# Kernel tuning notes

Measured on AMD Instinct MI355X. Metric: run time of the kernel, lower is better.

## Reference

```python
import jax, jax.numpy as jnp
import numpy as np

LN_EPS = 1e-5

def _ln(x, w, b):
    mu = jnp.mean(x, axis=-1, keepdims=True)
    var = jnp.var(x, axis=-1, keepdims=True)
    return (x - mu) * jax.lax.rsqrt(var + LN_EPS) * w + b

def setup_inputs() -> dict:
    key = jax.random.key(0)
    ks = jax.random.split(key, 16)
    B, T, N = 32, 1024, 77
    D, TD, TE = 512, 256, 2048
    s = lambda fan: 1.0 / np.sqrt(fan)
    return {
        "x": jax.random.normal(ks[0], (B, T, D), jnp.float32),
        "xf": jax.random.normal(ks[1], (B, N, TD), jnp.float32),
        "emb": jax.random.normal(ks[2], (B, TE), jnp.float32),
        "src_mask": jnp.ones((B, T), jnp.float32),
        "cond_type": jax.random.randint(ks[3], (B,), 0, 100, jnp.int64),
        "norm_w": jnp.ones((D,), jnp.float32),
        "norm_b": jnp.zeros((D,), jnp.float32),
        "tnorm_w": jnp.ones((TD,), jnp.float32),
        "tnorm_b": jnp.zeros((TD,), jnp.float32),
        "Wq": jax.random.normal(ks[4], (D, D), jnp.float32) * s(D),
        "bq": jnp.zeros((D,), jnp.float32),
        "Wk": jax.random.normal(ks[5], (D, TD), jnp.float32) * s(TD),
        "bk": jnp.zeros((D,), jnp.float32),
        "Wv": jax.random.normal(ks[6], (D, TD), jnp.float32) * s(TD),
        "bv": jnp.zeros((D,), jnp.float32),
        "emb_w": jax.random.normal(ks[7], (2 * D, TE), jnp.float32) * s(TE),
        "emb_b": jnp.zeros((2 * D,), jnp.float32),
        "snorm_w": jnp.ones((D,), jnp.float32),
        "snorm_b": jnp.zeros((D,), jnp.float32),
        "Wout": jax.random.normal(ks[8], (D, D), jnp.float32) * s(D),
        "bout": jnp.zeros((D,), jnp.float32),
    }

def reference(x, xf, emb, src_mask, cond_type,
              norm_w, norm_b, tnorm_w, tnorm_b,
              Wq, bq, Wk, bk, Wv, bv,
              emb_w, emb_b, snorm_w, snorm_b, Wout, bout):
    B, T, D = x.shape
    N = xf.shape[1]
    H = 8
    dh = D // H
    # projections (no 1/sqrt(dh) scaling, per original)
    q = (_ln(x, norm_w, norm_b) @ Wq.T + bq).reshape(B, T, H, dh)
    xf_n = _ln(xf, tnorm_w, tnorm_b)
    k = (xf_n @ Wk.T + bk).reshape(B, N, H, dh)
    # cond_type gating: text_cond_type = (cond_type % 10 > 0)
    tc = (cond_type % 10 > 0).astype(x.dtype)  # [B]
    bias = (1.0 - tc)[:, None, None, None] * -1000000.0  # [B,1,1,1]
    attn = jnp.einsum('bthd,bnhd->btnh', q, k) + bias
    attn = jax.nn.softmax(attn, axis=2)  # over keys N
    v = (xf_n @ Wv.T + bv) * tc[:, None, None]
    v = v.reshape(B, N, H, dh)
    y = jnp.einsum('btnh,bnhd->bthd', attn, v).reshape(B, T, D)
    # StylizationBlock: silu->linear on emb -> scale/shift, ln, silu->linear, residual
    e = jax.nn.silu(emb) @ emb_w.T + emb_b  # [B, 2D]
    scale, shift = jnp.split(e[:, None, :], 2, axis=2)  # [B,1,D] each
    h = _ln(y, snorm_w, snorm_b) * (1.0 + scale) + shift
    h = jax.nn.silu(h) @ Wout.T + bout
    return x + h
```

## Files before the change

### kernel.cpp

```cpp
#include <hip/hip_runtime.h>
#include <math.h>

#define B_   32
#define T_   1024
#define N_   77
#define D_   512
#define TD_  256
#define TE_  2048
#define H_   8
#define DH_  64

typedef short bf16x8 __attribute__((ext_vector_type(8)));
typedef float f32x4  __attribute__((ext_vector_type(4)));

__device__ __forceinline__ float sigmoidf_fast(float x) {
    return 1.0f / (1.0f + __expf(-x));
}

__device__ __forceinline__ unsigned short f2b(float f) {
    unsigned int u = __float_as_uint(f);
    unsigned int r = u + 0x7FFFu + ((u >> 16) & 1u);
    return (unsigned short)(r >> 16);
}

#define GL16(g, l) __builtin_amdgcn_global_load_lds(                         \
    (const __attribute__((address_space(1))) unsigned int*)(g),              \
    (__attribute__((address_space(3))) unsigned int*)(l), 16, 0, 0)

__global__ __launch_bounds__(256) void ln_xf_kernel(
    const float* __restrict__ x, const float* __restrict__ w, const float* __restrict__ b,
    unsigned short* __restrict__ outb)
{
    int row = blockIdx.x * 4 + (threadIdx.x >> 6);
    int lane = threadIdx.x & 63;
    const float* rp = x + (size_t)row * TD_ + lane * 4;
    float4 v = *(const float4*)rp;
    float s  = v.x + v.y + v.z + v.w;
    float ss = v.x*v.x + v.y*v.y + v.z*v.z + v.w*v.w;
    #pragma unroll
    for (int off = 32; off; off >>= 1) {
        s  += __shfl_xor(s, off);
        ss += __shfl_xor(ss, off);
    }
    float m = s * (1.f / TD_);
    float r = rsqrtf(ss * (1.f / TD_) - m * m + 1e-5f);
    float4 wv = *(const float4*)(w + lane * 4);
    float4 bv = *(const float4*)(b + lane * 4);
    ushort4 o;
    o.x = f2b((v.x - m) * r * wv.x + bv.x);
    o.y = f2b((v.y - m) * r * wv.y + bv.y);
    o.z = f2b((v.z - m) * r * wv.z + bv.z);
    o.w = f2b((v.w - m) * r * wv.w + bv.w);
    *(ushort4*)(outb + (size_t)row * TD_ + lane * 4) = o;
}

__global__ __launch_bounds__(256) void conv_weights_kernel(
    const float* __restrict__ Wq, const float* __restrict__ Wout,
    const float* __restrict__ Wk, const float* __restrict__ Wv,
    unsigned short* __restrict__ wqb, unsigned short* __restrict__ wob,
    unsigned short* __restrict__ wkvb)
{
    int bid = blockIdx.x;
    const float* src; unsigned short* dst;
    if (bid < 128)      { src = Wq;   dst = wqb; }
    else if (bid < 256) { src = Wout; dst = wob;               bid -= 128; }
    else if (bid < 320) { src = Wk;   dst = wkvb;              bid -= 256; }
    else                { src = Wv;   dst = wkvb + D_ * TD_;   bid -= 320; }
    int idx = (bid * 256 + threadIdx.x) * 8;
    float4 v0 = *(const float4*)(src + idx);
    float4 v1 = *(const float4*)(src + idx + 4);
    ushort4 o0 = {f2b(v0.x), f2b(v0.y), f2b(v0.z), f2b(v0.w)};
    ushort4 o1 = {f2b(v1.x), f2b(v1.y), f2b(v1.z), f2b(v1.w)};
    *(ushort4*)(dst + idx)     = o0;
    *(ushort4*)(dst + idx + 4) = o1;
}

__global__ __launch_bounds__(256) void kv_gemm_kernel(
    const unsigned short* __restrict__ Ab,
    const unsigned short* __restrict__ Wb,
    const float* __restrict__ bkp, const float* __restrict__ bvp,
    const int*   __restrict__ cond,
    unsigned short* __restrict__ kout, unsigned short* __restrict__ vout)
{
    constexpr int K = TD_;
    __shared__ __align__(16) unsigned short As[128 * 32];
    __shared__ __align__(16) unsigned short Bs[128 * 32];

    const int tid  = threadIdx.x;
    const int m0   = blockIdx.y * 128;
    const int n0   = blockIdx.x * 128;
    const int lane = tid & 63;
    const int w    = tid >> 6;
    const int l15  = lane & 15;
    const int quad = lane >> 4;
    const int wm   = (w >> 1) * 64;
    const int wn   = (w & 1) * 64;

    const int row_a = tid >> 2;
    const int col16 = tid & 3;

    f32x4 acc[4][4];
    #pragma unroll
    for (int i = 0; i < 4; i++)
        #pragma unroll
        for (int j = 0; j < 4; j++)
            acc[i][j] = (f32x4){0.f, 0.f, 0.f, 0.f};

    const char* gAbase = (const char*)Ab + ((size_t)(m0 + row_a) * K) * 2 + col16 * 16;
    const char* gBbase = (const char*)Wb + ((size_t)(n0 + row_a) * K) * 2 + col16 * 16;
    char* lA = (char*)As + tid * 16;
    char* lB = (char*)Bs + tid * 16;

    for (int k0 = 0; k0 < K; k0 += 32) {
        const char* gA = gAbase + k0 * 2;
        const char* gB = gBbase + k0 * 2;
        GL16(gA, lA);
        GL16(gA + (size_t)64 * K * 2, lA + 4096);
        GL16(gB, lB);
        GL16(gB + (size_t)64 * K * 2, lB + 4096);
        __syncthreads();

        bf16x8 af[4], bfr[4];
        #pragma unroll
        for (int i = 0; i < 4; i++)
            af[i] = *(const bf16x8*)&As[(wm + i * 16 + l15) * 32 + quad * 8];
        #pragma unroll
        for (int j = 0; j < 4; j++)
            bfr[j] = *(const bf16x8*)&Bs[(wn + j * 16 + l15) * 32 + quad * 8];
        #pragma unroll
        for (int i = 0; i < 4; i++)
            #pragma unroll
            for (int j = 0; j < 4; j++)
                acc[i][j] = __builtin_amdgcn_mfma_f32_16x16x32_bf16(af[i], bfr[j], acc[i][j], 0, 0, 0);
        __syncthreads();
    }

    #pragma unroll
    for (int i = 0; i < 4; i++) {
        int mbase = m0 + wm + i * 16 + quad * 4;
        #pragma unroll
        for (int j = 0; j < 4; j++) {
            int n = n0 + wn + j * 16 + l15;
            bool isv = n >= D_;
            int nn = isv ? n - D_ : n;
            float bn = isv ? bvp[nn] : bkp[nn];
            unsigned short* outp = isv ? vout : kout;
            #pragma unroll
            for (int r = 0; r < 4; r++) {
                int m = mbase + r;
                if (m >= B_ * N_) continue;
                float v = acc[i][j][r] + bn;
                if (isv) {
                    int bi = m / N_;
                    v = ((cond[bi] % 10) > 0) ? v : 0.f;
                }
                outp[(size_t)m * D_ + nn] = f2b(v);
            }
        }
    }
}

__global__ __launch_bounds__(256) void emb_gemm_kernel(
    const float* __restrict__ emb, const float* __restrict__ W,
    float* __restrict__ e)
{
    int wid = blockIdx.x * 4 + (threadIdx.x >> 6);
    int lane = threadIdx.x & 63;
    int ngrp = wid >> 3;
    int bgrp = wid & 7;

    float acc[4][4] = {};
    #pragma unroll 2
    for (int it = 0; it < 8; it++) {
        int k = (it * 64 + lane) * 4;
        float4 sv[4], wv[4];
        #pragma unroll
        for (int bi = 0; bi < 4; bi++) {
            float4 t = *(const float4*)&emb[(size_t)(bgrp * 4 + bi) * TE_ + k];
            t.x *= sigmoidf_fast(t.x);
            t.y *= sigmoidf_fast(t.y);
            t.z *= sigmoidf_fast(t.z);
            t.w *= sigmoidf_fast(t.w);
            sv[bi] = t;
        }
        #pragma unroll
        for (int ni = 0; ni < 4; ni++)
            wv[ni] = *(const float4*)&W[(size_t)(ngrp * 4 + ni) * TE_ + k];
        #pragma unroll
        for (int bi = 0; bi < 4; bi++)
            #pragma unroll
            for (int ni = 0; ni < 4; ni++) {
                acc[bi][ni] = fmaf(sv[bi].x, wv[ni].x, acc[bi][ni]);
                acc[bi][ni] = fmaf(sv[bi].y, wv[ni].y, acc[bi][ni]);
                acc[bi][ni] = fmaf(sv[bi].z, wv[ni].z, acc[bi][ni]);
                acc[bi][ni] = fmaf(sv[bi].w, wv[ni].w, acc[bi][ni]);
            }
    }
    #pragma unroll
    for (int bi = 0; bi < 4; bi++)
        #pragma unroll
        for (int ni = 0; ni < 4; ni++) {
            float a = acc[bi][ni];
            #pragma unroll
            for (int off = 32; off; off >>= 1) a += __shfl_xor(a, off);
            if (lane == 0)
                e[(size_t)(bgrp * 4 + bi) * 1024 + ngrp * 4 + ni] = a;
        }
}

__global__ __launch_bounds__(256) void prep_q_kernel(
    const float* __restrict__ x, const float* __restrict__ w, const float* __restrict__ b,
    unsigned short* __restrict__ outb)
{
    int row = blockIdx.x * 4 + (threadIdx.x >> 6);
    int lane = threadIdx.x & 63;
    const float* rp = x + (size_t)row * D_ + lane * 8;
    float4 v0 = *(const float4*)rp;
    float4 v1 = *(const float4*)(rp + 4);
    float s  = v0.x + v0.y + v0.z + v0.w + v1.x + v1.y + v1.z + v1.w;
    float ss = v0.x*v0.x + v0.y*v0.y + v0.z*v0.z + v0.w*v0.w
             + v1.x*v1.x + v1.y*v1.y + v1.z*v1.z + v1.w*v1.w;
    #pragma unroll
    for (int off = 32; off; off >>= 1) {
        s  += __shfl_xor(s, off);
        ss += __shfl_xor(ss, off);
    }
    float m = s * (1.f / D_);
    float r = rsqrtf(ss * (1.f / D_) - m * m + 1e-5f);
    float4 w0 = *(const float4*)(w + lane * 8);
    float4 w1 = *(const float4*)(w + lane * 8 + 4);
    float4 b0 = *(const float4*)(b + lane * 8);
    float4 b1 = *(const float4*)(b + lane * 8 + 4);
    ushort4 o0, o1;
    o0.x = f2b((v0.x - m) * r * w0.x + b0.x);
    o0.y = f2b((v0.y - m) * r * w0.y + b0.y);
    o0.z = f2b((v0.z - m) * r * w0.z + b0.z);
    o0.w = f2b((v0.w - m) * r * w0.w + b0.w);
    o1.x = f2b((v1.x - m) * r * w1.x + b1.x);
    o1.y = f2b((v1.y - m) * r * w1.y + b1.y);
    o1.z = f2b((v1.z - m) * r * w1.z + b1.z);
    o1.w = f2b((v1.w - m) * r * w1.w + b1.w);
    unsigned short* op = outb + (size_t)row * D_ + lane * 8;
    *(ushort4*)op       = o0;
    *(ushort4*)(op + 4) = o1;
}

__global__ __launch_bounds__(256) void prep_h_kernel(
    const float* __restrict__ y, const float* __restrict__ w, const float* __restrict__ b,
    const float* __restrict__ e, const float* __restrict__ emb_b,
    unsigned short* __restrict__ outb)
{
    int row = blockIdx.x * 4 + (threadIdx.x >> 6);
    int lane = threadIdx.x & 63;
    int bb = row >> 10;
    const float* rp = y + (size_t)row * D_ + lane * 8;
    float4 v0 = *(const float4*)rp;
    float4 v1 = *(const float4*)(rp + 4);
    float s  = v0.x + v0.y + v0.z + v0.w + v1.x + v1.y + v1.z + v1.w;
    float ss = v0.x*v0.x + v0.y*v0.y + v0.z*v0.z + v0.w*v0.w
             + v1.x*v1.x + v1.y*v1.y + v1.z*v1.z + v1.w*v1.w;
    #pragma unroll
    for (int off = 32; off; off >>= 1) {
        s  += __shfl_xor(s, off);
        ss += __shfl_xor(ss, off);
    }
    float m = s * (1.f / D_);
    float r = rsqrtf(ss * (1.f / D_) - m * m + 1e-5f);
    float4 w0 = *(const float4*)(w + lane * 8);
    float4 w1 = *(const float4*)(w + lane * 8 + 4);
    float4 b0 = *(const float4*)(b + lane * 8);
    float4 b1 = *(const float4*)(b + lane * 8 + 4);
    const float* ep = e + (size_t)bb * 1024 + lane * 8;
    float4 sc0 = *(const float4*)ep;
    float4 sc1 = *(const float4*)(ep + 4);
    float4 sh0 = *(const float4*)(ep + 512);
    float4 sh1 = *(const float4*)(ep + 512 + 4);
    float4 eb0 = *(const float4*)(emb_b + lane * 8);
    float4 eb1 = *(const float4*)(emb_b + lane * 8 + 4);
    float4 fb0 = *(const float4*)(emb_b + 512 + lane * 8);
    float4 fb1 = *(const float4*)(emb_b + 512 + lane * 8 + 4);
    sc0.x += eb0.x; sc0.y += eb0.y; sc0.z += eb0.z; sc0.w += eb0.w;
    sc1.x += eb1.x; sc1.y += eb1.y; sc1.z += eb1.z; sc1.w += eb1.w;
    sh0.x += fb0.x; sh0.y += fb0.y; sh0.z += fb0.z; sh0.w += fb0.w;
    sh1.x += fb1.x; sh1.y += fb1.y; sh1.z += fb1.z; sh1.w += fb1.w;
    float hv[8];
    hv[0] = ((v0.x - m) * r * w0.x + b0.x) * (1.f + sc0.x) + sh0.x;
    hv[1] = ((v0.y - m) * r * w0.y + b0.y) * (1.f + sc0.y) + sh0.y;
    hv[2] = ((v0.z - m) * r * w0.z + b0.z) * (1.f + sc0.z) + sh0.z;
    hv[3] = ((v0.w - m) * r * w0.w + b0.w) * (1.f + sc0.w) + sh0.w;
    hv[4] = ((v1.x - m) * r * w1.x + b1.x) * (1.f + sc1.x) + sh1.x;
    hv[5] = ((v1.y - m) * r * w1.y + b1.y) * (1.f + sc1.y) + sh1.y;
    hv[6] = ((v1.z - m) * r * w1.z + b1.z) * (1.f + sc1.z) + sh1.z;
    hv[7] = ((v1.w - m) * r * w1.w + b1.w) * (1.f + sc1.w) + sh1.w;
    ushort4 o0, o1;
    o0.x = f2b(hv[0] * sigmoidf_fast(hv[0]));
    o0.y = f2b(hv[1] * sigmoidf_fast(hv[1]));
    o0.z = f2b(hv[2] * sigmoidf_fast(hv[2]));
    o0.w = f2b(hv[3] * sigmoidf_fast(hv[3]));
    o1.x = f2b(hv[4] * sigmoidf_fast(hv[4]));
    o1.y = f2b(hv[5] * sigmoidf_fast(hv[5]));
    o1.z = f2b(hv[6] * sigmoidf_fast(hv[6]));
    o1.w = f2b(hv[7] * sigmoidf_fast(hv[7]));
    unsigned short* op = outb + (size_t)row * D_ + lane * 8;
    *(ushort4*)op       = o0;
    *(ushort4*)(op + 4) = o1;
}

template <int RESID, int OUTBF>
__global__ __launch_bounds__(256) void gemm_bf16_kernel(
    const unsigned short* __restrict__ Ab,
    const unsigned short* __restrict__ Wb,
    const float* __restrict__ bias,
    const float* __restrict__ resid,
    void* __restrict__ Cv)
{
    constexpr int K = 512;
    __shared__ __align__(16) unsigned short As[128 * 32];
    __shared__ __align__(16) unsigned short Bs[128 * 32];

    const int tid  = threadIdx.x;
    const int m0   = blockIdx.y * 128;
    const int n0   = blockIdx.x * 128;
    const int lane = tid & 63;
    const int w    = tid >> 6;
    const int l15  = lane & 15;
    const int quad = lane >> 4;
    const int wm   = (w >> 1) * 64;
    const int wn   = (w & 1) * 64;

    const int row_a = tid >> 2;
    const int col16 = tid & 3;

    f32x4 acc[4][4];
    #pragma unroll
    for (int i = 0; i < 4; i++)
        #pragma unroll
        for (int j = 0; j < 4; j++)
            acc[i][j] = (f32x4){0.f, 0.f, 0.f, 0.f};

    const char* gAbase = (const char*)Ab + ((size_t)(m0 + row_a) * K) * 2 + col16 * 16;
    const char* gBbase = (const char*)Wb + ((size_t)(n0 + row_a) * K) * 2 + col16 * 16;
    char* lA = (char*)As + tid * 16;
    char* lB = (char*)Bs + tid * 16;

    for (int k0 = 0; k0 < K; k0 += 32) {
        const char* gA = gAbase + k0 * 2;
        const char* gB = gBbase + k0 * 2;
        GL16(gA, lA);
        GL16(gA + (size_t)64 * K * 2, lA + 4096);
        GL16(gB, lB);
        GL16(gB + (size_t)64 * K * 2, lB + 4096);
        __syncthreads();

        bf16x8 af[4], bfr[4];
        #pragma unroll
        for (int i = 0; i < 4; i++)
            af[i] = *(const bf16x8*)&As[(wm + i * 16 + l15) * 32 + quad * 8];
        #pragma unroll
        for (int j = 0; j < 4; j++)
            bfr[j] = *(const bf16x8*)&Bs[(wn + j * 16 + l15) * 32 + quad * 8];
        #pragma unroll
        for (int i = 0; i < 4; i++)
            #pragma unroll
            for (int j = 0; j < 4; j++)
                acc[i][j] = __builtin_amdgcn_mfma_f32_16x16x32_bf16(af[i], bfr[j], acc[i][j], 0, 0, 0);
        __syncthreads();
    }

    float* C = (float*)Cv;
    unsigned short* Cb = (unsigned short*)Cv;
    #pragma unroll
    for (int i = 0; i < 4; i++) {
        int mbase = m0 + wm + i * 16 + quad * 4;
        #pragma unroll
        for (int j = 0; j < 4; j++) {
            int n = n0 + wn + j * 16 + l15;
            float bn = bias[n];
            #pragma unroll
            for (int r = 0; r < 4; r++) {
                size_t off = (size_t)(mbase + r) * 512 + n;
                float v = acc[i][j][r] + bn;
                if (RESID) v += resid[off];
                if (OUTBF) Cb[off] = f2b(v);
                else       C[off]  = v;
            }
        }
    }
}

#define KS2   0
#define VT2   5760
#define PS2   11904
#define SMEM2 18560

__global__ __launch_bounds__(256) void attn_mfma2_kernel(
    const unsigned short* __restrict__ qb,
    const unsigned short* __restrict__ kb,
    const unsigned short* __restrict__ vb,
    float* __restrict__ yout)
{
    __shared__ __align__(16) unsigned short smem[SMEM2];

    const int tid = threadIdx.x;
    const int t0 = blockIdx.x * 64;
    const int h  = blockIdx.y;
    const int b  = blockIdx.z;

    const int lane = tid & 63;
    const int w    = tid >> 6;
    const int l15  = lane & 15;
    const int quad = lane >> 4;
    const int koff = quad * 8;
    const int mrow = w * 16 + l15;

    const unsigned short* qrow = qb + ((size_t)(b * T_ + t0 + mrow)) * D_ + h * 64 + koff;
    bf16x8 aq0 = *(const bf16x8*)qrow;
    bf16x8 aq1 = *(const bf16x8*)(qrow + 32);

    const unsigned short* kbase = kb + ((size_t)(b * N_)) * D_ + h * 64;
    #pragma unroll
    for (int i = 0; i < 3; i++) {
        int idx = tid + i * 256;
        if (idx < 640) {
            int row = idx >> 3, c8 = idx & 7;
            bf16x8 v = (bf16x8){0, 0, 0, 0, 0, 0, 0, 0};
            if (row < N_) v = *(const bf16x8*)(kbase + (size_t)row * D_ + c8 * 8);
            *(bf16x8*)&smem[KS2 + row * 72 + c8 * 8] = v;
        }
    }
    const unsigned short* vbase = vb + ((size_t)(b * N_)) * D_ + h * 64;
    #pragma unroll
    for (int i = 0; i < 3; i++) {
        int idx = tid + i * 256;
        if (idx < 616) {
            int n = idx >> 3, c8 = idx & 7;
            bf16x8 v = *(const bf16x8*)(vbase + (size_t)n * D_ + c8 * 8);
            int cn = n >> 3, wn = n & 7;
            #pragma unroll
            for (int j = 0; j < 8; j++) {
                int d = c8 * 8 + j;
                int s2 = (j ^ c8) & 3;
                smem[VT2 + d * 96 + ((cn ^ s2) << 3) + wn] = v[j];
            }
        }
    }
    if (tid < 128) {
        int d = tid >> 1, c = 10 + (tid & 1);
        int s2 = (d ^ (d >> 3)) & 3;
        *(bf16x8*)&smem[VT2 + d * 96 + ((c ^ s2) << 3)] = (bf16x8){0, 0, 0, 0, 0, 0, 0, 0};
    }
    {
        int d = tid >> 2, t = tid & 3;
        if (t < 3) {
            int s2 = (d ^ (d >> 3)) & 3;
            smem[VT2 + d * 96 + ((9 ^ s2) << 3) + 5 + t] = 0;
        }
    }
    #pragma unroll
    for (int i = 0; i < 4; i++) {
        int idx = tid + i * 256;
        int row = idx >> 4, col = 80 + (idx & 15);
        smem[PS2 + row * 104 + col] = 0;
    }
    __syncthreads();

    float s[5][4];
    #pragma unroll
    for (int nt = 0; nt < 5; nt++) {
        bf16x8 bk0 = *(const bf16x8*)&smem[KS2 + (nt * 16 + l15) * 72 + koff];
        bf16x8 bk1 = *(const bf16x8*)&smem[KS2 + (nt * 16 + l15) * 72 + 32 + koff];
        f32x4 c = {0.f, 0.f, 0.f, 0.f};
        c = __builtin_amdgcn_mfma_f32_16x16x32_bf16(aq0, bk0, c, 0, 0, 0);
        c = __builtin_amdgcn_mfma_f32_16x16x32_bf16(aq1, bk1, c, 0, 0, 0);
        #pragma unroll
        for (int r = 0; r < 4; r++) s[nt][r] = c[r];
    }
    if (l15 >= N_ - 64) {
        #pragma unroll
        for (int r = 0; r < 4; r++) s[4][r] = -1e30f;
    }
    float li[4];
    #pragma unroll
    for (int r = 0; r < 4; r++) {
        float m = s[0][r];
        #pragma unroll
        for (int nt = 1; nt < 5; nt++) m = fmaxf(m, s[nt][r]);
        m = fmaxf(m, __shfl_xor(m, 1));
        m = fmaxf(m, __shfl_xor(m, 2));
        m = fmaxf(m, __shfl_xor(m, 4));
        m = fmaxf(m, __shfl_xor(m, 8));
        float l = 0.f;
        #pragma unroll
        for (int nt = 0; nt < 5; nt++) {
            float ev = __expf(s[nt][r] - m);
            s[nt][r] = ev;
            l += ev;
        }
        l += __shfl_xor(l, 1);
        l += __shfl_xor(l, 2);
        l += __shfl_xor(l, 4);
        l += __shfl_xor(l, 8);
        li[r] = 1.f / l;
    }
    #pragma unroll
    for (int r = 0; r < 4; r++) {
        int prow = w * 16 + quad * 4 + r;
        #pragma unroll
        for (int nt = 0; nt < 5; nt++) {
            smem[PS2 + prow * 104 + nt * 16 + l15] = f2b(s[nt][r] * li[r]);
        }
    }

    bf16x8 pa0 = *(const bf16x8*)&smem[PS2 + mrow * 104 + 0  + koff];
    bf16x8 pa1 = *(const bf16x8*)&smem[PS2 + mrow * 104 + 32 + koff];
    bf16x8 pa2 = *(const bf16x8*)&smem[PS2 + mrow * 104 + 64 + koff];

    float* obase = yout + ((size_t)(b * T_ + t0 + w * 16)) * D_ + h * 64;
    #pragma unroll
    for (int dt = 0; dt < 4; dt++) {
        int drow = dt * 16 + l15;
        int s2 = (drow ^ (drow >> 3)) & 3;
        bf16x8 bv0 = *(const bf16x8*)&smem[VT2 + drow * 96 + (((0 + quad) ^ s2) << 3)];
        bf16x8 bv1 = *(const bf16x8*)&smem[VT2 + drow * 96 + (((4 + quad) ^ s2) << 3)];
        bf16x8 bv2 = *(const bf16x8*)&smem[VT2 + drow * 96 + (((8 + quad) ^ s2) << 3)];
        f32x4 c = {0.f, 0.f, 0.f, 0.f};
        c = __builtin_amdgcn_mfma_f32_16x16x32_bf16(pa0, bv0, c, 0, 0, 0);
        c = __builtin_amdgcn_mfma_f32_16x16x32_bf16(pa1, bv1, c, 0, 0, 0);
        c = __builtin_amdgcn_mfma_f32_16x16x32_bf16(pa2, bv2, c, 0, 0, 0);
        #pragma unroll
        for (int r = 0; r < 4; r++) {
            obase[(size_t)(quad * 4 + r) * D_ + dt * 16 + l15] = c[r];
        }
    }
}

extern "C" void kernel_launch(void* const* d_in, const int* in_sizes, int n_in,
                              void* d_out, int out_size, void* d_ws, size_t ws_size,
                              hipStream_t stream)
{
    const float* x       = (const float*)d_in[0];
    const float* xf      = (const float*)d_in[1];
    const float* emb     = (const float*)d_in[2];
    const int*   cond    = (const int*)d_in[4];
    const float* norm_w  = (const float*)d_in[5];
    const float* norm_b  = (const float*)d_in[6];
    const float* tnorm_w = (const float*)d_in[7];
    const float* tnorm_b = (const float*)d_in[8];
    const float* Wq      = (const float*)d_in[9];
    const float* bq      = (const float*)d_in[10];
    const float* Wk      = (const float*)d_in[11];
    const float* bk      = (const float*)d_in[12];
    const float* Wv      = (const float*)d_in[13];
    const float* bv      = (const float*)d_in[14];
    const float* emb_w   = (const float*)d_in[15];
    const float* emb_b   = (const float*)d_in[16];
    const float* snorm_w = (const float*)d_in[17];
    const float* snorm_b = (const float*)d_in[18];
    const float* Wout    = (const float*)d_in[19];
    const float* bout    = (const float*)d_in[20];
    float* out = (float*)d_out;

    float* ws = (float*)d_ws;
    float* qy   = ws;
    float* ebuf = qy + (size_t)B_ * T_ * D_;
    unsigned short* u = (unsigned short*)(ebuf + (size_t)B_ * 2 * D_);
    unsigned short* xfnb = u;  u += (size_t)2560 * TD_;
    unsigned short* kb16 = u;  u += (size_t)B_ * N_ * D_;
    unsigned short* vb16 = u;  u += (size_t)B_ * N_ * D_;
    unsigned short* abh  = u;  u += (size_t)B_ * T_ * D_;
    unsigned short* wqb  = u;  u += (size_t)D_ * D_;
    unsigned short* wob  = u;  u += (size_t)D_ * D_;
    unsigned short* wkvb = u;  u += (size_t)2 * D_ * TD_;
    unsigned short* qb = (unsigned short*)d_out;

    const int BT = B_ * T_;
    const int BN = B_ * N_;

    ln_xf_kernel<<<BN / 4, 256, 0, stream>>>(xf, tnorm_w, tnorm_b, xfnb);
    conv_weights_kernel<<<384, 256, 0, stream>>>(Wq, Wout, Wk, Wv, wqb, wob, wkvb);
    {
        dim3 grid(1024 / 128, 2560 / 128);
        kv_gemm_kernel<<<grid, 256, 0, stream>>>(xfnb, wkvb, bk, bv, cond, kb16, vb16);
    }
    prep_q_kernel<<<BT / 4, 256, 0, stream>>>(x, norm_w, norm_b, abh);
    {
        dim3 grid(D_ / 128, BT / 128);
        gemm_bf16_kernel<0, 1><<<grid, 256, 0, stream>>>(abh, wqb, bq, nullptr, qb);
    }
    emb_gemm_kernel<<<512, 256, 0, stream>>>(emb, emb_w, ebuf);
    {
        dim3 grid(T_ / 64, H_, B_);
        attn_mfma2_kernel<<<grid, 256, 0, stream>>>(qb, kb16, vb16, qy);
    }
    prep_h_kernel<<<BT / 4, 256, 0, stream>>>(qy, snorm_w, snorm_b, ebuf, emb_b, abh);
    {
        dim3 grid(D_ / 128, BT / 128);
        gemm_bf16_kernel<1, 0><<<grid, 256, 0, stream>>>(abh, wob, bout, x, out);
    }
}
```

Measured before the change: 316.2 us.

## Store attention output as bf16 and double-buffer swizzled 128x64 GEMM tiles

The attention kernel now writes its output in bf16 rather than fp32, and prep_h reads bf16. This halves the intermediate y traffic, at the cost of some precision before the layer norm. The bf16 GEMM moves to 128x64 tiles with double-buffered LDS staging and an XOR swizzle, overlapping global-to-LDS loads with MFMA work and reducing bank conflicts. The smaller tile also doubles the number of blocks, which should help occupancy and load balance.

```diff
diff --git a/kernel.cpp b/kernel.cpp
--- a/kernel.cpp
+++ b/kernel.cpp
@@ -21,6 +21,10 @@
     unsigned int u = __float_as_uint(f);
     unsigned int r = u + 0x7FFFu + ((u >> 16) & 1u);
     return (unsigned short)(r >> 16);
+}
+
+__device__ __forceinline__ float b2f(short us) {
+    return __uint_as_float(((unsigned int)(unsigned short)us) << 16);
 }
 
 #define GL16(g, l) __builtin_amdgcn_global_load_lds(                         \
@@ -246,19 +250,21 @@
 }
 
 __global__ __launch_bounds__(256) void prep_h_kernel(
-    const float* __restrict__ y, const float* __restrict__ w, const float* __restrict__ b,
+    const unsigned short* __restrict__ y, const float* __restrict__ w, const float* __restrict__ b,
     const float* __restrict__ e, const float* __restrict__ emb_b,
     unsigned short* __restrict__ outb)
 {
     int row = blockIdx.x * 4 + (threadIdx.x >> 6);
     int lane = threadIdx.x & 63;
     int bb = row >> 10;
-    const float* rp = y + (size_t)row * D_ + lane * 8;
-    float4 v0 = *(const float4*)rp;
-    float4 v1 = *(const float4*)(rp + 4);
-    float s  = v0.x + v0.y + v0.z + v0.w + v1.x + v1.y + v1.z + v1.w;
-    float ss = v0.x*v0.x + v0.y*v0.y + v0.z*v0.z + v0.w*v0.w
-             + v1.x*v1.x + v1.y*v1.y + v1.z*v1.z + v1.w*v1.w;
+    const unsigned short* rp = y + (size_t)row * D_ + lane * 8;
+    bf16x8 yv = *(const bf16x8*)rp;
+    float v[8];
+    #pragma unroll
+    for (int k2 = 0; k2 < 8; k2++) v[k2] = b2f(yv[k2]);
+    float s = 0.f, ss = 0.f;
+    #pragma unroll
+    for (int k2 = 0; k2 < 8; k2++) { s += v[k2]; ss += v[k2] * v[k2]; }
     #pragma unroll
     for (int off = 32; off; off >>= 1) {
         s  += __shfl_xor(s, off);
@@ -270,6 +276,8 @@
     float4 w1 = *(const float4*)(w + lane * 8 + 4);
     float4 b0 = *(const float4*)(b + lane * 8);
     float4 b1 = *(const float4*)(b + lane * 8 + 4);
+    float wa[8] = {w0.x, w0.y, w0.z, w0.w, w1.x, w1.y, w1.z, w1.w};
+    float ba[8] = {b0.x, b0.y, b0.z, b0.w, b1.x, b1.y, b1.z, b1.w};
     const float* ep = e + (size_t)bb * 1024 + lane * 8;
     float4 sc0 = *(const float4*)ep;
     float4 sc1 = *(const float4*)(ep + 4);
@@ -279,28 +287,19 @@
     float4 eb1 = *(const float4*)(emb_b + lane * 8 + 4);
     float4 fb0 = *(const float4*)(emb_b + 512 + lane * 8);
     float4 fb1 = *(const float4*)(emb_b + 512 + lane * 8 + 4);
-    sc0.x += eb0.x; sc0.y += eb0.y; sc0.z += eb0.z; sc0.w += eb0.w;
-    sc1.x += eb1.x; sc1.y += eb1.y; sc1.z += eb1.z; sc1.w += eb1.w;
-    sh0.x += fb0.x; sh0.y += fb0.y; sh0.z += fb0.z; sh0.w += fb0.w;
-    sh1.x += fb1.x; sh1.y += fb1.y; sh1.z += fb1.z; sh1.w += fb1.w;
-    float hv[8];
-    hv[0] = ((v0.x - m) * r * w0.x + b0.x) * (1.f + sc0.x) + sh0.x;
-    hv[1] = ((v0.y - m) * r * w0.y + b0.y) * (1.f + sc0.y) + sh0.y;
-    hv[2] = ((v0.z - m) * r * w0.z + b0.z) * (1.f + sc0.z) + sh0.z;
-    hv[3] = ((v0.w - m) * r * w0.w + b0.w) * (1.f + sc0.w) + sh0.w;
-    hv[4] = ((v1.x - m) * r * w1.x + b1.x) * (1.f + sc1.x) + sh1.x;
-    hv[5] = ((v1.y - m) * r * w1.y + b1.y) * (1.f + sc1.y) + sh1.y;
-    hv[6] = ((v1.z - m) * r * w1.z + b1.z) * (1.f + sc1.z) + sh1.z;
-    hv[7] = ((v1.w - m) * r * w1.w + b1.w) * (1.f + sc1.w) + sh1.w;
+    float sca[8] = {sc0.x + eb0.x, sc0.y + eb0.y, sc0.z + eb0.z, sc0.w + eb0.w,
+                    sc1.x + eb1.x, sc1.y + eb1.y, sc1.z + eb1.z, sc1.w + eb1.w};
+    float sha[8] = {sh0.x + fb0.x, sh0.y + fb0.y, sh0.z + fb0.z, sh0.w + fb0.w,
+                    sh1.x + fb1.x, sh1.y + fb1.y, sh1.z + fb1.z, sh1.w + fb1.w};
     ushort4 o0, o1;
-    o0.x = f2b(hv[0] * sigmoidf_fast(hv[0]));
-    o0.y = f2b(hv[1] * sigmoidf_fast(hv[1]));
-    o0.z = f2b(hv[2] * sigmoidf_fast(hv[2]));
-    o0.w = f2b(hv[3] * sigmoidf_fast(hv[3]));
-    o1.x = f2b(hv[4] * sigmoidf_fast(hv[4]));
-    o1.y = f2b(hv[5] * sigmoidf_fast(hv[5]));
-    o1.z = f2b(hv[6] * sigmoidf_fast(hv[6]));
-    o1.w = f2b(hv[7] * sigmoidf_fast(hv[7]));
+    unsigned short oa[8];
+    #pragma unroll
+    for (int k2 = 0; k2 < 8; k2++) {
+        float hv = ((v[k2] - m) * r * wa[k2] + ba[k2]) * (1.f + sca[k2]) + sha[k2];
+        oa[k2] = f2b(hv * sigmoidf_fast(hv));
+    }
+    o0.x = oa[0]; o0.y = oa[1]; o0.z = oa[2]; o0.w = oa[3];
+    o1.x = oa[4]; o1.y = oa[5]; o1.z = oa[6]; o1.w = oa[7];
     unsigned short* op = outb + (size_t)row * D_ + lane * 8;
     *(ushort4*)op       = o0;
     *(ushort4*)(op + 4) = o1;
@@ -315,66 +314,90 @@
     void* __restrict__ Cv)
 {
     constexpr int K = 512;
-    __shared__ __align__(16) unsigned short As[128 * 32];
-    __shared__ __align__(16) unsigned short Bs[128 * 32];
+    __shared__ __align__(16) unsigned short As[2][128 * 32];
+    __shared__ __align__(16) unsigned short Bs[2][64 * 32];
 
     const int tid  = threadIdx.x;
     const int m0   = blockIdx.y * 128;
-    const int n0   = blockIdx.x * 128;
+    const int n0   = blockIdx.x * 64;
     const int lane = tid & 63;
     const int w    = tid >> 6;
     const int l15  = lane & 15;
     const int quad = lane >> 4;
-    const int wm   = (w >> 1) * 64;
-    const int wn   = (w & 1) * 64;
-
-    const int row_a = tid >> 2;
-    const int col16 = tid & 3;
-
-    f32x4 acc[4][4];
-    #pragma unroll
-    for (int i = 0; i < 4; i++)
+    const int wm   = w * 32;
+
+    const int row_s = tid >> 2;
+    const int ck    = (tid & 3) ^ (row_s & 3);
+
+    f32x4 acc[2][4];
+    #pragma unroll
+    for (int i = 0; i < 2; i++)
         #pragma unroll
         for (int j = 0; j < 4; j++)
             acc[i][j] = (f32x4){0.f, 0.f, 0.f, 0.f};
 
-    const char* gAbase = (const char*)Ab + ((size_t)(m0 + row_a) * K) * 2 + col16 * 16;
-    const char* gBbase = (const char*)Wb + ((size_t)(n0 + row_a) * K) * 2 + col16 * 16;
-    char* lA = (char*)As + tid * 16;
-    char* lB = (char*)Bs + tid * 16;
-
-    for (int k0 = 0; k0 < K; k0 += 32) {
-        const char* gA = gAbase + k0 * 2;
-        const char* gB = gBbase + k0 * 2;
-        GL16(gA, lA);
-        GL16(gA + (size_t)64 * K * 2, lA + 4096);
-        GL16(gB, lB);
-        GL16(gB + (size_t)64 * K * 2, lB + 4096);
+    const char* gA = (const char*)Ab + ((size_t)(m0 + row_s) * K) * 2 + ck * 16;
+    const char* gB = (const char*)Wb + ((size_t)(n0 + row_s) * K) * 2 + ck * 16;
+    const size_t gA2 = (size_t)64 * K * 2;
+    char* lA = (char*)&As[0][0] + tid * 16;
+    char* lB = (char*)&Bs[0][0] + tid * 16;
+
+#define STAGE_G(s, buf) do {                                                  \
+        const char* pA_ = gA + (s) * 64;                                      \
+        GL16(pA_,       lA + (buf) * 8192);                                   \
+        GL16(pA_ + gA2, lA + (buf) * 8192 + 4096);                            \
+        GL16(gB + (s) * 64, lB + (buf) * 4096);                               \
+    } while (0)
+
+    const int sc = (quad ^ (l15 & 3)) << 3;
+    bf16x8 af0, af1, bf0, bf1, bf2, bf3;
+
+#define LOADF_G(buf) do {                                                     \
+        af0 = *(const bf16x8*)&As[buf][(wm      + l15) * 32 + sc];            \
+        af1 = *(const bf16x8*)&As[buf][(wm + 16 + l15) * 32 + sc];            \
+        bf0 = *(const bf16x8*)&Bs[buf][(      l15) * 32 + sc];                \
+        bf1 = *(const bf16x8*)&Bs[buf][(16 + l15) * 32 + sc];                 \
+        bf2 = *(const bf16x8*)&Bs[buf][(32 + l15) * 32 + sc];                 \
+        bf3 = *(const bf16x8*)&Bs[buf][(48 + l15) * 32 + sc];                 \
+    } while (0)
+
+#define MFMA_G() do {                                                         \
+        acc[0][0] = __builtin_amdgcn_mfma_f32_16x16x32_bf16(af0, bf0, acc[0][0], 0, 0, 0); \
+        acc[0][1] = __builtin_amdgcn_mfma_f32_16x16x32_bf16(af0, bf1, acc[0][1], 0, 0, 0); \
+        acc[0][2] = __builtin_amdgcn_mfma_f32_16x16x32_bf16(af0, bf2, acc[0][2], 0, 0, 0); \
+        acc[0][3] = __builtin_amdgcn_mfma_f32_16x16x32_bf16(af0, bf3, acc[0][3], 0, 0, 0); \
+        acc[1][0] = __builtin_amdgcn_mfma_f32_16x16x32_bf16(af1, bf0, acc[1][0], 0, 0, 0); \
+        acc[1][1] = __builtin_amdgcn_mfma_f32_16x16x32_bf16(af1, bf1, acc[1][1], 0, 0, 0); \
+        acc[1][2] = __builtin_amdgcn_mfma_f32_16x16x32_bf16(af1, bf2, acc[1][2], 0, 0, 0); \
+        acc[1][3] = __builtin_amdgcn_mfma_f32_16x16x32_bf16(af1, bf3, acc[1][3], 0, 0, 0); \
+    } while (0)
+
+    STAGE_G(0, 0);
+    __syncthreads();
+
+    #pragma unroll 1
+    for (int t = 0; t < 8; t++) {
+        LOADF_G(0);
+        STAGE_G(2 * t + 1, 1);
+        MFMA_G();
         __syncthreads();
-
-        bf16x8 af[4], bfr[4];
-        #pragma unroll
-        for (int i = 0; i < 4; i++)
-            af[i] = *(const bf16x8*)&As[(wm + i * 16 + l15) * 32 + quad * 8];
-        #pragma unroll
-        for (int j = 0; j < 4; j++)
-            bfr[j] = *(const bf16x8*)&Bs[(wn + j * 16 + l15) * 32 + quad * 8];
-        #pragma unroll
-        for (int i = 0; i < 4; i++)
-            #pragma unroll
-            for (int j = 0; j < 4; j++)
-                acc[i][j] = __builtin_amdgcn_mfma_f32_16x16x32_bf16(af[i], bfr[j], acc[i][j], 0, 0, 0);
+        LOADF_G(1);
+        if (t < 7) STAGE_G(2 * t + 2, 0);
+        MFMA_G();
         __syncthreads();
     }
+#undef STAGE_G
+#undef LOADF_G
+#undef MFMA_G
 
     float* C = (float*)Cv;
     unsigned short* Cb = (unsigned short*)Cv;
     #pragma unroll
-    for (int i = 0; i < 4; i++) {
+    for (int i = 0; i < 2; i++) {
         int mbase = m0 + wm + i * 16 + quad * 4;
         #pragma unroll
         for (int j = 0; j < 4; j++) {
-            int n = n0 + wn + j * 16 + l15;
+            int n = n0 + j * 16 + l15;
             float bn = bias[n];
             #pragma unroll
             for (int r = 0; r < 4; r++) {
@@ -397,7 +420,7 @@
     const unsigned short* __restrict__ qb,
     const unsigned short* __restrict__ kb,
     const unsigned short* __restrict__ vb,
-    float* __restrict__ yout)
+    unsigned short* __restrict__ yout)
 {
     __shared__ __align__(16) unsigned short smem[SMEM2];
 
@@ -515,7 +538,7 @@
     bf16x8 pa1 = *(const bf16x8*)&smem[PS2 + mrow * 104 + 32 + koff];
     bf16x8 pa2 = *(const bf16x8*)&smem[PS2 + mrow * 104 + 64 + koff];
 
-    float* obase = yout + ((size_t)(b * T_ + t0 + w * 16)) * D_ + h * 64;
+    unsigned short* obase = yout + ((size_t)(b * T_ + t0 + w * 16)) * D_ + h * 64;
     #pragma unroll
     for (int dt = 0; dt < 4; dt++) {
         int drow = dt * 16 + l15;
@@ -529,7 +552,7 @@
         c = __builtin_amdgcn_mfma_f32_16x16x32_bf16(pa2, bv2, c, 0, 0, 0);
         #pragma unroll
         for (int r = 0; r < 4; r++) {
-            obase[(size_t)(quad * 4 + r) * D_ + dt * 16 + l15] = c[r];
+            obase[(size_t)(quad * 4 + r) * D_ + dt * 16 + l15] = f2b(c[r]);
         }
     }
 }
@@ -561,9 +584,9 @@
     float* out = (float*)d_out;
 
     float* ws = (float*)d_ws;
-    float* qy   = ws;
-    float* ebuf = qy + (size_t)B_ * T_ * D_;
+    float* ebuf = ws;
     unsigned short* u = (unsigned short*)(ebuf + (size_t)B_ * 2 * D_);
+    unsigned short* qyb  = u;  u += (size_t)B_ * T_ * D_;
     unsigned short* xfnb = u;  u += (size_t)2560 * TD_;
     unsigned short* kb16 = u;  u += (size_t)B_ * N_ * D_;
     unsigned short* vb16 = u;  u += (size_t)B_ * N_ * D_;
@@ -584,17 +607,17 @@
     }
     prep_q_kernel<<<BT / 4, 256, 0, stream>>>(x, norm_w, norm_b, abh);
     {
-        dim3 grid(D_ / 128, BT / 128);
+        dim3 grid(D_ / 64, BT / 128);
         gemm_bf16_kernel<0, 1><<<grid, 256, 0, stream>>>(abh, wqb, bq, nullptr, qb);
     }
     emb_gemm_kernel<<<512, 256, 0, stream>>>(emb, emb_w, ebuf);
     {
         dim3 grid(T_ / 64, H_, B_);
-        attn_mfma2_kernel<<<grid, 256, 0, stream>>>(qb, kb16, vb16, qy);
-    }
-    prep_h_kernel<<<BT / 4, 256, 0, stream>>>(qy, snorm_w, snorm_b, ebuf, emb_b, abh);
+        attn_mfma2_kernel<<<grid, 256, 0, stream>>>(qb, kb16, vb16, qyb);
+    }
+    prep_h_kernel<<<BT / 4, 256, 0, stream>>>(qyb, snorm_w, snorm_b, ebuf, emb_b, abh);
     {
-        dim3 grid(D_ / 128, BT / 128);
+        dim3 grid(D_ / 64, BT / 128);
         gemm_bf16_kernel<1, 0><<<grid, 256, 0, stream>>>(abh, wob, bout, x, out);
     }
 }
```

After: 341.6 us. 8.0% more time.
